# Kernel optimization log

Hardware: AMD Instinct MI355X
Metric: run time of the kernel (lower is better)

The kernel has to match this reference:

```python
import jax, jax.numpy as jnp
import numpy as np

IN_FEATURES = 1024
OUT_FEATURES = 1280
K = 16  # intermediate_features
B_EXTRA = OUT_FEATURES - IN_FEATURES  # 256
N = 256


def setup_inputs() -> dict:
    key = jax.random.key(0)
    k1, k2 = jax.random.split(key)
    x = jax.random.normal(k1, (N, IN_FEATURES), dtype=jnp.float32)
    T = jax.random.normal(k2, (IN_FEATURES, B_EXTRA, K), dtype=jnp.float32) * 0.02
    return {"x": x, "T": T}


def reference(x, T):
    # M: (N, B_extra, K)
    M = jnp.einsum('ni,ibk->nbk', x, T)
    # pairwise L1 over K: (N, N, B_extra)
    l1 = jnp.abs(M[:, None, :, :] - M[None, :, :, :]).sum(axis=3)
    # sum over the other-sample axis, subtract self term exp(0)=1
    out = jnp.exp(-l1).sum(axis=0) - 1.0  # (N, B_extra)
    return jnp.concatenate([x, out], axis=1)  # (N, OUT_FEATURES)
```

## Files before the change

### kernel.cpp

```cpp
#include <hip/hip_runtime.h>
#include <hip/hip_fp16.h>
#include <hip/hip_bf16.h>

#define NB 256
#define IN_F 1024
#define BEX 256
#define KD 16
#define NJ 4096
#define OUT_F 1280

typedef short bf16x8 __attribute__((ext_vector_type(8)));
typedef float f32x4 __attribute__((ext_vector_type(4)));

__device__ inline unsigned short f2bf(float f) {
    __hip_bfloat16 h = __float2bfloat16(f);
    return *reinterpret_cast<unsigned short*>(&h);
}

__device__ inline void cp16(const void* g, void* l) {
    __builtin_amdgcn_global_load_lds((const __attribute__((address_space(1))) void*)g,
                                     (__attribute__((address_space(3))) void*)l, 16, 0, 0);
}

__global__ __launch_bounds__(256) void k_copy_x(const float* __restrict__ x,
                                                float* __restrict__ out,
                                                unsigned short* __restrict__ x_bf) {
    const int r = blockIdx.x;
    const int t = threadIdx.x;
    float4 v = *(const float4*)(x + (size_t)r * IN_F + t * 4);
    *(float4*)(out + (size_t)r * OUT_F + t * 4) = v;
    ushort4 o;
    o.x = f2bf(v.x); o.y = f2bf(v.y); o.z = f2bf(v.z); o.w = f2bf(v.w);
    *(ushort4*)(x_bf + (size_t)r * IN_F + t * 4) = o;
    if (t < 64)
        *(float4*)(out + (size_t)r * OUT_F + IN_F + t * 4) = make_float4(-1.f, -1.f, -1.f, -1.f);
}

__global__ __launch_bounds__(256) void k_transpose(const float* __restrict__ T,
                                                   unsigned short* __restrict__ Tt) {
    __shared__ float tile[32][33];
    const int i0 = blockIdx.y * 32;
    const int j0 = blockIdx.x * 32;
    const int t = threadIdx.x;
    {
        const int r = t >> 3, cg = (t & 7) << 2;
        float4 v = *(const float4*)(T + (size_t)(i0 + r) * NJ + j0 + cg);
        tile[r][cg + 0] = v.x; tile[r][cg + 1] = v.y;
        tile[r][cg + 2] = v.z; tile[r][cg + 3] = v.w;
    }
    __syncthreads();
    const int jr = t >> 3, ig = (t & 7) << 2;
    ushort4 o;
    o.x = f2bf(tile[ig + 0][jr]);
    o.y = f2bf(tile[ig + 1][jr]);
    o.z = f2bf(tile[ig + 2][jr]);
    o.w = f2bf(tile[ig + 3][jr]);
    *(ushort4*)(Tt + (size_t)(j0 + jr) * IN_F + i0 + ig) = o;
}

__global__ __launch_bounds__(256) void k_gemm(const unsigned short* __restrict__ A,
                                              const unsigned short* __restrict__ B,
                                              __half* __restrict__ M2h) {
    __shared__ unsigned short lds[4][64 * 128];
    const int t = threadIdx.x;
    const int w = t >> 6, l = t & 63;
    const int n0 = blockIdx.y * 64;
    const int j0 = blockIdx.x * 64;

    const unsigned short* aA[4];
    const unsigned short* aB[4];
    int lofs[4];
    #pragma unroll
    for (int p = 0; p < 4; ++p) {
        int s = t + p * 256;
        int r = s >> 4;
        int kg = (s & 15) ^ (r & 15);
        aA[p] = A + (size_t)(n0 + r) * IN_F + kg * 8;
        aB[p] = B + (size_t)(j0 + r) * IN_F + kg * 8;
        lofs[p] = s * 8;
    }

    f32x4 acc[2][2];
    #pragma unroll
    for (int i = 0; i < 2; ++i)
        #pragma unroll
        for (int j = 0; j < 2; ++j)
            acc[i][j] = (f32x4){0.f, 0.f, 0.f, 0.f};

    #pragma unroll
    for (int p = 0; p < 4; ++p) cp16(aA[p], &lds[0][lofs[p]]);
    #pragma unroll
    for (int p = 0; p < 4; ++p) cp16(aB[p], &lds[1][lofs[p]]);

    const int rowA0 = ((w & 1) * 32 + (l & 15)) * 128;
    const int rowA1 = rowA0 + 16 * 128;
    const int rowB0 = (((w >> 1) & 1) * 32 + (l & 15)) * 128;
    const int rowB1 = rowB0 + 16 * 128;

    for (int s = 0; s < 8; ++s) {
        __syncthreads();
        if (s < 7) {
            const int k0 = (s + 1) * 128;
            const int bsel = ((s + 1) & 1) * 2;
            #pragma unroll
            for (int p = 0; p < 4; ++p) cp16(aA[p] + k0, &lds[bsel + 0][lofs[p]]);
            #pragma unroll
            for (int p = 0; p < 4; ++p) cp16(aB[p] + k0, &lds[bsel + 1][lofs[p]]);
        }
        const unsigned short* La = lds[(s & 1) * 2 + 0];
        const unsigned short* Lb = lds[(s & 1) * 2 + 1];
        #pragma unroll
        for (int kk = 0; kk < 4; ++kk) {
            const int kg = kk * 4 + (l >> 4);
            const int ks = (kg ^ (l & 15)) * 8;
            bf16x8 a0 = *(const bf16x8*)&La[rowA0 + ks];
            bf16x8 a1 = *(const bf16x8*)&La[rowA1 + ks];
            bf16x8 b0 = *(const bf16x8*)&Lb[rowB0 + ks];
            bf16x8 b1 = *(const bf16x8*)&Lb[rowB1 + ks];
            acc[0][0] = __builtin_amdgcn_mfma_f32_16x16x32_bf16(a0, b0, acc[0][0], 0, 0, 0);
            acc[0][1] = __builtin_amdgcn_mfma_f32_16x16x32_bf16(a0, b1, acc[0][1], 0, 0, 0);
            acc[1][0] = __builtin_amdgcn_mfma_f32_16x16x32_bf16(a1, b0, acc[1][0], 0, 0, 0);
            acc[1][1] = __builtin_amdgcn_mfma_f32_16x16x32_bf16(a1, b1, acc[1][1], 0, 0, 0);
        }
    }

    const int col = l & 15;
    #pragma unroll
    for (int nt = 0; nt < 2; ++nt) {
        #pragma unroll
        for (int jt = 0; jt < 2; ++jt) {
            const int jc = j0 + ((w >> 1) & 1) * 32 + jt * 16 + col;
            const int b = jc >> 4;
            const int k = jc & 15;
            __half* base = M2h + (size_t)b * (NB * KD) + k;
            #pragma unroll
            for (int r = 0; r < 4; ++r) {
                const int n = n0 + (w & 1) * 32 + nt * 16 + (l >> 4) * 4 + r;
                base[n * KD] = __float2half(acc[nt][jt][r]);
            }
        }
    }
}

__global__ __launch_bounds__(256) void k_pairwise(const __half* __restrict__ M2h,
                                                  float* __restrict__ out) {
    __shared__ __half lds[2][64][16];
    const int bpair = blockIdx.x;
    const int mc = blockIdx.y;
    const int t = threadIdx.x;
    const int half = t >> 7;
    const int b = bpair * 2 + half;
    const int tl = t & 127;

    {
        const int bb = t >> 7, idx = t & 127, row = idx >> 1, h = idx & 1;
        float4 v = *(const float4*)(M2h + (size_t)(bpair * 2 + bb) * (NB * KD)
                                    + (mc * 64 + row) * KD + h * 8);
        *(float4*)&lds[bb][row][h * 8] = v;
    }

    union U { float4 f; __half2 h[4]; };
    U q0a, q0b, q1a, q1b;
    {
        const __half* q0p = M2h + (size_t)b * (NB * KD) + tl * KD;
        const __half* q1p = M2h + (size_t)b * (NB * KD) + (tl + 128) * KD;
        q0a.f = *(const float4*)(q0p);     q0b.f = *(const float4*)(q0p + 8);
        q1a.f = *(const float4*)(q1p);     q1b.f = *(const float4*)(q1p + 8);
    }
    __syncthreads();

    float e0 = 0.f, e1 = 0.f;
    #pragma unroll 2
    for (int m = 0; m < 64; ++m) {
        U pa, pb;
        pa.f = *(const float4*)&lds[half][m][0];
        pb.f = *(const float4*)&lds[half][m][8];

        {
            __half2 s0 = __hadd2(__habs2(__hsub2(q0a.h[0], pa.h[0])), __habs2(__hsub2(q0a.h[1], pa.h[1])));
            __half2 s1 = __hadd2(__habs2(__hsub2(q0a.h[2], pa.h[2])), __habs2(__hsub2(q0a.h[3], pa.h[3])));
            __half2 s2 = __hadd2(__habs2(__hsub2(q0b.h[0], pb.h[0])), __habs2(__hsub2(q0b.h[1], pb.h[1])));
            __half2 s3 = __hadd2(__habs2(__hsub2(q0b.h[2], pb.h[2])), __habs2(__hsub2(q0b.h[3], pb.h[3])));
            __half2 sA = __hadd2(s0, s1);
            __half2 sB = __hadd2(s2, s3);
            float2 fa = __half22float2(sA);
            float2 fb = __half22float2(sB);
            float l1 = (fa.x + fa.y) + (fb.x + fb.y);
            e0 += __expf(-l1);
        }
        {
            __half2 s0 = __hadd2(__habs2(__hsub2(q1a.h[0], pa.h[0])), __habs2(__hsub2(q1a.h[1], pa.h[1])));
            __half2 s1 = __hadd2(__habs2(__hsub2(q1a.h[2], pa.h[2])), __habs2(__hsub2(q1a.h[3], pa.h[3])));
            __half2 s2 = __hadd2(__habs2(__hsub2(q1b.h[0], pb.h[0])), __habs2(__hsub2(q1b.h[1], pb.h[1])));
            __half2 s3 = __hadd2(__habs2(__hsub2(q1b.h[2], pb.h[2])), __habs2(__hsub2(q1b.h[3], pb.h[3])));
            __half2 sA = __hadd2(s0, s1);
            __half2 sB = __hadd2(s2, s3);
            float2 fa = __half22float2(sA);
            float2 fb = __half22float2(sB);
            float l1 = (fa.x + fa.y) + (fb.x + fb.y);
            e1 += __expf(-l1);
        }
    }
    atomicAdd(&out[(size_t)tl * OUT_F + IN_F + b], e0);
    atomicAdd(&out[(size_t)(tl + 128) * OUT_F + IN_F + b], e1);
}

extern "C" void kernel_launch(void* const* d_in, const int* in_sizes, int n_in,
                              void* d_out, int out_size, void* d_ws, size_t ws_size,
                              hipStream_t stream) {
    const float* x = (const float*)d_in[0];
    const float* T = (const float*)d_in[1];
    float* out = (float*)d_out;

    char* ws = (char*)d_ws;
    unsigned short* x_bf = (unsigned short*)ws;
    unsigned short* Tt   = (unsigned short*)(ws + (1u << 19));
    __half* M2h          = (__half*)(ws + (1u << 19) + (1u << 23));

    k_copy_x<<<dim3(256), dim3(256), 0, stream>>>(x, out, x_bf);
    k_transpose<<<dim3(128, 32), dim3(256), 0, stream>>>(T, Tt);
    k_gemm<<<dim3(64, 4), dim3(256), 0, stream>>>(x_bf, Tt, M2h);
    k_pairwise<<<dim3(128, 4), dim3(256), 0, stream>>>(M2h, out);
}
```

Before: 103.5 us.

## Merge prep kernels and retile pairwise L1 with fdot2 reductions

Fuses the x copy/convert kernel and the T transpose kernel into one launch, saving a kernel launch. Restructures the pairwise kernel so each block handles one feature b and half of the m rows, and each thread holds 4 query rows in registers. This raises register-level reuse of each LDS row load. The L1 reduction now masks off sign bits and uses packed fp16 fdot2 accumulating into fp32, with an LDS partial reduction that halves the number of atomics. Costs are higher register pressure and an extra syncthreads.

```diff
diff --git a/kernel.cpp b/kernel.cpp
--- a/kernel.cpp
+++ b/kernel.cpp
@@ -11,6 +11,7 @@
 
 typedef short bf16x8 __attribute__((ext_vector_type(8)));
 typedef float f32x4 __attribute__((ext_vector_type(4)));
+typedef _Float16 h2 __attribute__((ext_vector_type(2)));
 
 __device__ inline unsigned short f2bf(float f) {
     __hip_bfloat16 h = __float2bfloat16(f);
@@ -22,40 +23,42 @@
                                      (__attribute__((address_space(3))) void*)l, 16, 0, 0);
 }
 
-__global__ __launch_bounds__(256) void k_copy_x(const float* __restrict__ x,
-                                                float* __restrict__ out,
-                                                unsigned short* __restrict__ x_bf) {
-    const int r = blockIdx.x;
+__global__ __launch_bounds__(256) void k_prep(const float* __restrict__ x,
+                                              const float* __restrict__ T,
+                                              float* __restrict__ out,
+                                              unsigned short* __restrict__ x_bf,
+                                              unsigned short* __restrict__ Tt) {
+    const int bid = blockIdx.x;
     const int t = threadIdx.x;
-    float4 v = *(const float4*)(x + (size_t)r * IN_F + t * 4);
-    *(float4*)(out + (size_t)r * OUT_F + t * 4) = v;
-    ushort4 o;
-    o.x = f2bf(v.x); o.y = f2bf(v.y); o.z = f2bf(v.z); o.w = f2bf(v.w);
-    *(ushort4*)(x_bf + (size_t)r * IN_F + t * 4) = o;
-    if (t < 64)
-        *(float4*)(out + (size_t)r * OUT_F + IN_F + t * 4) = make_float4(-1.f, -1.f, -1.f, -1.f);
-}
-
-__global__ __launch_bounds__(256) void k_transpose(const float* __restrict__ T,
-                                                   unsigned short* __restrict__ Tt) {
-    __shared__ float tile[32][33];
-    const int i0 = blockIdx.y * 32;
-    const int j0 = blockIdx.x * 32;
-    const int t = threadIdx.x;
-    {
-        const int r = t >> 3, cg = (t & 7) << 2;
-        float4 v = *(const float4*)(T + (size_t)(i0 + r) * NJ + j0 + cg);
-        tile[r][cg + 0] = v.x; tile[r][cg + 1] = v.y;
-        tile[r][cg + 2] = v.z; tile[r][cg + 3] = v.w;
-    }
-    __syncthreads();
-    const int jr = t >> 3, ig = (t & 7) << 2;
-    ushort4 o;
-    o.x = f2bf(tile[ig + 0][jr]);
-    o.y = f2bf(tile[ig + 1][jr]);
-    o.z = f2bf(tile[ig + 2][jr]);
-    o.w = f2bf(tile[ig + 3][jr]);
-    *(ushort4*)(Tt + (size_t)(j0 + jr) * IN_F + i0 + ig) = o;
+    if (bid < 4096) {
+        __shared__ float tile[32][33];
+        const int j0 = (bid & 127) * 32;
+        const int i0 = (bid >> 7) * 32;
+        {
+            const int r = t >> 3, cg = (t & 7) << 2;
+            float4 v = *(const float4*)(T + (size_t)(i0 + r) * NJ + j0 + cg);
+            tile[r][cg + 0] = v.x; tile[r][cg + 1] = v.y;
+            tile[r][cg + 2] = v.z; tile[r][cg + 3] = v.w;
+        }
+        __syncthreads();
+        const int jr = t >> 3, ig = (t & 7) << 2;
+        ushort4 o;
+        o.x = f2bf(tile[ig + 0][jr]);
+        o.y = f2bf(tile[ig + 1][jr]);
+        o.z = f2bf(tile[ig + 2][jr]);
+        o.w = f2bf(tile[ig + 3][jr]);
+        *(ushort4*)(Tt + (size_t)(j0 + jr) * IN_F + i0 + ig) = o;
+    } else {
+        const int r = bid - 4096;
+        float4 v = *(const float4*)(x + (size_t)r * IN_F + t * 4);
+        *(float4*)(out + (size_t)r * OUT_F + t * 4) = v;
+        ushort4 o;
+        o.x = f2bf(v.x); o.y = f2bf(v.y); o.z = f2bf(v.z); o.w = f2bf(v.w);
+        *(ushort4*)(x_bf + (size_t)r * IN_F + t * 4) = o;
+        if (t < 64)
+            *(float4*)(out + (size_t)r * OUT_F + IN_F + t * 4) =
+                make_float4(-1.f, -1.f, -1.f, -1.f);
+    }
 }
 
 __global__ __launch_bounds__(256) void k_gemm(const unsigned short* __restrict__ A,
@@ -142,67 +145,61 @@
     }
 }
 
+union U8 { float4 f4[2]; h2 h[8]; };
+
 __global__ __launch_bounds__(256) void k_pairwise(const __half* __restrict__ M2h,
                                                   float* __restrict__ out) {
-    __shared__ __half lds[2][64][16];
-    const int bpair = blockIdx.x;
-    const int mc = blockIdx.y;
+    __shared__ __half rows[128 * KD];
+    __shared__ float part[256 * 4];
+    const int b = blockIdx.x;
+    const int mh = blockIdx.y;
     const int t = threadIdx.x;
-    const int half = t >> 7;
-    const int b = bpair * 2 + half;
-    const int tl = t & 127;
-
-    {
-        const int bb = t >> 7, idx = t & 127, row = idx >> 1, h = idx & 1;
-        float4 v = *(const float4*)(M2h + (size_t)(bpair * 2 + bb) * (NB * KD)
-                                    + (mc * 64 + row) * KD + h * 8);
-        *(float4*)&lds[bb][row][h * 8] = v;
-    }
-
-    union U { float4 f; __half2 h[4]; };
-    U q0a, q0b, q1a, q1b;
-    {
-        const __half* q0p = M2h + (size_t)b * (NB * KD) + tl * KD;
-        const __half* q1p = M2h + (size_t)b * (NB * KD) + (tl + 128) * KD;
-        q0a.f = *(const float4*)(q0p);     q0b.f = *(const float4*)(q0p + 8);
-        q1a.f = *(const float4*)(q1p);     q1b.f = *(const float4*)(q1p + 8);
+    const int qg = t & 63, ms = t >> 6;
+    const __half* Mb = M2h + (size_t)b * (NB * KD);
+
+    ((float4*)rows)[t] = ((const float4*)(Mb + mh * 128 * KD))[t];
+
+    U8 q[4];
+    #pragma unroll
+    for (int r = 0; r < 4; ++r) {
+        const __half* qp = Mb + (qg * 4 + r) * KD;
+        q[r].f4[0] = *(const float4*)(qp);
+        q[r].f4[1] = *(const float4*)(qp + 8);
     }
     __syncthreads();
 
-    float e0 = 0.f, e1 = 0.f;
+    const h2 one = {(_Float16)1.0f, (_Float16)1.0f};
+    float e[4] = {0.f, 0.f, 0.f, 0.f};
+
     #pragma unroll 2
-    for (int m = 0; m < 64; ++m) {
-        U pa, pb;
-        pa.f = *(const float4*)&lds[half][m][0];
-        pb.f = *(const float4*)&lds[half][m][8];
-
-        {
-            __half2 s0 = __hadd2(__habs2(__hsub2(q0a.h[0], pa.h[0])), __habs2(__hsub2(q0a.h[1], pa.h[1])));
-            __half2 s1 = __hadd2(__habs2(__hsub2(q0a.h[2], pa.h[2])), __habs2(__hsub2(q0a.h[3], pa.h[3])));
-            __half2 s2 = __hadd2(__habs2(__hsub2(q0b.h[0], pb.h[0])), __habs2(__hsub2(q0b.h[1], pb.h[1])));
-            __half2 s3 = __hadd2(__habs2(__hsub2(q0b.h[2], pb.h[2])), __habs2(__hsub2(q0b.h[3], pb.h[3])));
-            __half2 sA = __hadd2(s0, s1);
-            __half2 sB = __hadd2(s2, s3);
-            float2 fa = __half22float2(sA);
-            float2 fb = __half22float2(sB);
-            float l1 = (fa.x + fa.y) + (fb.x + fb.y);
-            e0 += __expf(-l1);
-        }
-        {
-            __half2 s0 = __hadd2(__habs2(__hsub2(q1a.h[0], pa.h[0])), __habs2(__hsub2(q1a.h[1], pa.h[1])));
-            __half2 s1 = __hadd2(__habs2(__hsub2(q1a.h[2], pa.h[2])), __habs2(__hsub2(q1a.h[3], pa.h[3])));
-            __half2 s2 = __hadd2(__habs2(__hsub2(q1b.h[0], pb.h[0])), __habs2(__hsub2(q1b.h[1], pb.h[1])));
-            __half2 s3 = __hadd2(__habs2(__hsub2(q1b.h[2], pb.h[2])), __habs2(__hsub2(q1b.h[3], pb.h[3])));
-            __half2 sA = __hadd2(s0, s1);
-            __half2 sB = __hadd2(s2, s3);
-            float2 fa = __half22float2(sA);
-            float2 fb = __half22float2(sB);
-            float l1 = (fa.x + fa.y) + (fb.x + fb.y);
-            e1 += __expf(-l1);
-        }
-    }
-    atomicAdd(&out[(size_t)tl * OUT_F + IN_F + b], e0);
-    atomicAdd(&out[(size_t)(tl + 128) * OUT_F + IN_F + b], e1);
+    for (int m = 0; m < 32; ++m) {
+        U8 p;
+        const __half* rp = rows + (ms * 32 + m) * KD;
+        p.f4[0] = *(const float4*)(rp);
+        p.f4[1] = *(const float4*)(rp + 8);
+        #pragma unroll
+        for (int r = 0; r < 4; ++r) {
+            float l0 = 0.f, l1 = 0.f;
+            #pragma unroll
+            for (int i = 0; i < 8; i += 2) {
+                h2 d0 = q[r].h[i] - p.h[i];
+                h2 d1 = q[r].h[i + 1] - p.h[i + 1];
+                unsigned u0 = (*(unsigned*)&d0) & 0x7FFF7FFFu;
+                unsigned u1 = (*(unsigned*)&d1) & 0x7FFF7FFFu;
+                l0 = __builtin_amdgcn_fdot2(*(h2*)&u0, one, l0, false);
+                l1 = __builtin_amdgcn_fdot2(*(h2*)&u1, one, l1, false);
+            }
+            e[r] += __expf(-(l0 + l1));
+        }
+    }
+
+    #pragma unroll
+    for (int r = 0; r < 4; ++r)
+        part[(qg * 4 + r) * 4 + ms] = e[r];
+    __syncthreads();
+
+    float4 p4 = ((const float4*)part)[t];
+    atomicAdd(&out[(size_t)t * OUT_F + IN_F + b], p4.x + p4.y + p4.z + p4.w);
 }
 
 extern "C" void kernel_launch(void* const* d_in, const int* in_sizes, int n_in,
@@ -217,8 +214,7 @@
     unsigned short* Tt   = (unsigned short*)(ws + (1u << 19));
     __half* M2h          = (__half*)(ws + (1u << 19) + (1u << 23));
 
-    k_copy_x<<<dim3(256), dim3(256), 0, stream>>>(x, out, x_bf);
-    k_transpose<<<dim3(128, 32), dim3(256), 0, stream>>>(T, Tt);
+    k_prep<<<dim3(4352), dim3(256), 0, stream>>>(x, T, out, x_bf, Tt);
     k_gemm<<<dim3(64, 4), dim3(256), 0, stream>>>(x_bf, Tt, M2h);
-    k_pairwise<<<dim3(128, 4), dim3(256), 0, stream>>>(M2h, out);
-}
+    k_pairwise<<<dim3(256, 2), dim3(256), 0, stream>>>(M2h, out);
+}
```

Result: faster. 96.31 us (median of 2 runs) (-6.9%).
